# Optimization experiments

Measured on AMD Instinct MI355X. Metric: run time of the kernel, lower is better.

Reference implementation:

```python
import jax, jax.numpy as jnp
import numpy as np
import math

D = 64  # block size == head dim


def _sdpa(q, k, v):
    # q,k,v: [..., n, d]
    d = q.shape[-1]
    scores = jnp.einsum('...nd,...md->...nm', q / math.sqrt(d), k)
    probs = jax.nn.softmax(scores, axis=-1)
    return jnp.einsum('...nm,...md->...nd', probs, v)


def setup_inputs() -> dict:
    key = jax.random.key(0)
    kq, kk, kv = jax.random.split(key, 3)
    B, H, N = 4, 16, 4128  # N = 64*64 + 32 -> nonzero remainder
    q = jax.random.normal(kq, (B, H, N, D), dtype=jnp.float32)
    k = jax.random.normal(kk, (B, H, N, D), dtype=jnp.float32)
    v = jax.random.normal(kv, (B, H, N, D), dtype=jnp.float32)
    return {'q': q, 'k': k, 'v': v}


def reference(q, k, v):
    B, H, N, d = q.shape
    ND = d * (N // d)          # length covered by full DxD blocks
    h = H * (ND // d)          # total number of block-heads
    Q = q[:, :, :ND, :].reshape(B, h, d, d)
    K = k[:, :, :ND, :].reshape(B, h, d, d)
    V = v[:, :, :ND, :].reshape(B, h, d, d)
    attn_main = _sdpa(Q, K, V).reshape(B, H, ND, d)
    attn_rem = _sdpa(q[:, :, ND:, :], k[:, :, ND:, :], v[:, :, ND:, :])
    return jnp.concatenate([attn_main, attn_rem], axis=-2)
```

## Files before the change

### kernel.cpp

```cpp
#include <hip/hip_runtime.h>
#include <math.h>

#define STRH 72

typedef __attribute__((ext_vector_type(8))) short short8;
typedef __attribute__((ext_vector_type(4))) float f32x4;
typedef __attribute__((ext_vector_type(4))) short short4v;

__device__ __forceinline__ void split2(float x, unsigned short& h, unsigned short& l) {
  unsigned u = __float_as_uint(x);
  unsigned hb = (u + 0x7FFFu + ((u >> 16) & 1u)) & 0xFFFF0000u;
  h = (unsigned short)(hb >> 16);
  float r = x - __uint_as_float(hb);
  unsigned v = __float_as_uint(r);
  l = (unsigned short)((v + 0x7FFFu + ((v >> 16) & 1u)) >> 16);
}

__global__ __launch_bounds__(256, 4) void bda_kernel(
    const float* __restrict__ qg,
    const float* __restrict__ kg,
    const float* __restrict__ vg,
    float* __restrict__ og,
    int N, int nblk, int rem) {
  __shared__ unsigned short Ah[64 * STRH];
  __shared__ unsigned short Al[64 * STRH];
  __shared__ unsigned short Bh[64 * STRH];
  __shared__ unsigned short Bl[64 * STRH];

  const int wg  = blockIdx.x;
  const int blk = wg % nblk;
  const int bh  = wg / nblk;
  const int nrows = (blk == nblk - 1 && rem != 0) ? rem : 64;
  const size_t base = ((size_t)bh * (size_t)N + (size_t)blk * 64) * 64;

  const int t    = threadIdx.x;
  const int lane = t & 63;
  const int w    = t >> 6;

#pragma unroll
  for (int rnd = 0; rnd < 4; ++rnd) {
    const int e = (t << 2) + (rnd << 10);
    const int row = e >> 6, col = e & 63;
    float4 qv = make_float4(0.f, 0.f, 0.f, 0.f);
    float4 kv = qv;
    if (row < nrows) {
      qv = *(const float4*)(qg + base + e);
      kv = *(const float4*)(kg + base + e);
    }
    unsigned short qh[4], ql[4], kh[4], kl[4];
    split2(qv.x, qh[0], ql[0]); split2(qv.y, qh[1], ql[1]);
    split2(qv.z, qh[2], ql[2]); split2(qv.w, qh[3], ql[3]);
    split2(kv.x, kh[0], kl[0]); split2(kv.y, kh[1], kl[1]);
    split2(kv.z, kh[2], kl[2]); split2(kv.w, kh[3], kl[3]);
    const int a = row * STRH + col;
    *(short4v*)&Ah[a] = (short4v){(short)qh[0], (short)qh[1], (short)qh[2], (short)qh[3]};
    *(short4v*)&Al[a] = (short4v){(short)ql[0], (short)ql[1], (short)ql[2], (short)ql[3]};
    *(short4v*)&Bh[a] = (short4v){(short)kh[0], (short)kh[1], (short)kh[2], (short)kh[3]};
    *(short4v*)&Bl[a] = (short4v){(short)kl[0], (short)kl[1], (short)kl[2], (short)kl[3]};
  }

  const int vd  = t & 63;
  const int vkb = (t >> 6) * 16;
  float vr[16];
#pragma unroll
  for (int i = 0; i < 16; ++i) {
    const int k = vkb + i;
    vr[i] = (k < nrows) ? vg[base + (size_t)k * 64 + vd] : 0.f;
  }

  __syncthreads();

  const int colb = lane & 15;
  const int kofs = (lane >> 4) * 8;
  const int arow = 16 * w + colb;

  f32x4 acc[4];
#pragma unroll
  for (int i = 0; i < 4; ++i) acc[i] = (f32x4){0.f, 0.f, 0.f, 0.f};

#pragma unroll
  for (int ks = 0; ks < 2; ++ks) {
    const int kb = ks * 32 + kofs;
    const short8 ah = *(const short8*)&Ah[arow * STRH + kb];
    const short8 al = *(const short8*)&Al[arow * STRH + kb];
#pragma unroll
    for (int nt = 0; nt < 4; ++nt) {
      const int brow = 16 * nt + colb;
      const short8 bhv = *(const short8*)&Bh[brow * STRH + kb];
      const short8 blv = *(const short8*)&Bl[brow * STRH + kb];
      acc[nt] = __builtin_amdgcn_mfma_f32_16x16x32_bf16(al, bhv, acc[nt], 0, 0, 0);
      acc[nt] = __builtin_amdgcn_mfma_f32_16x16x32_bf16(ah, blv, acc[nt], 0, 0, 0);
      acc[nt] = __builtin_amdgcn_mfma_f32_16x16x32_bf16(ah, bhv, acc[nt], 0, 0, 0);
    }
  }

  const int rquad = (lane >> 4) * 4;
#pragma unroll
  for (int r = 0; r < 4; ++r) {
    const int grow = 16 * w + rquad + r;
    float s[4];
#pragma unroll
    for (int nt = 0; nt < 4; ++nt) {
      const int col = 16 * nt + colb;
      s[nt] = (col < nrows) ? acc[nt][r] * 0.125f : -1e30f;
    }
    float m = fmaxf(fmaxf(s[0], s[1]), fmaxf(s[2], s[3]));
    m = fmaxf(m, __shfl_xor(m, 1));
    m = fmaxf(m, __shfl_xor(m, 2));
    m = fmaxf(m, __shfl_xor(m, 4));
    m = fmaxf(m, __shfl_xor(m, 8));
    float p[4];
    float lsum = 0.f;
#pragma unroll
    for (int nt = 0; nt < 4; ++nt) {
      p[nt] = __expf(s[nt] - m);
      lsum += p[nt];
    }
    lsum += __shfl_xor(lsum, 1);
    lsum += __shfl_xor(lsum, 2);
    lsum += __shfl_xor(lsum, 4);
    lsum += __shfl_xor(lsum, 8);
    const float inv = 1.f / lsum;
#pragma unroll
    for (int nt = 0; nt < 4; ++nt) {
      unsigned short hh, ll;
      split2(p[nt] * inv, hh, ll);
      Ah[grow * STRH + 16 * nt + colb] = hh;
      Al[grow * STRH + 16 * nt + colb] = ll;
    }
  }

  __syncthreads();

#pragma unroll
  for (int c = 0; c < 4; ++c) {
    unsigned short h4[4], l4[4];
#pragma unroll
    for (int i = 0; i < 4; ++i) split2(vr[4 * c + i], h4[i], l4[i]);
    const int a = vd * STRH + vkb + 4 * c;
    *(short4v*)&Bh[a] = (short4v){(short)h4[0], (short)h4[1], (short)h4[2], (short)h4[3]};
    *(short4v*)&Bl[a] = (short4v){(short)l4[0], (short)l4[1], (short)l4[2], (short)l4[3]};
  }
  __syncthreads();

  f32x4 oacc[4];
#pragma unroll
  for (int i = 0; i < 4; ++i) oacc[i] = (f32x4){0.f, 0.f, 0.f, 0.f};

#pragma unroll
  for (int ks = 0; ks < 2; ++ks) {
    const int kb = ks * 32 + kofs;
    const short8 ph = *(const short8*)&Ah[arow * STRH + kb];
    const short8 pl = *(const short8*)&Al[arow * STRH + kb];
#pragma unroll
    for (int nt = 0; nt < 4; ++nt) {
      const int vrow = 16 * nt + colb;
      const short8 vh = *(const short8*)&Bh[vrow * STRH + kb];
      const short8 vl = *(const short8*)&Bl[vrow * STRH + kb];
      oacc[nt] = __builtin_amdgcn_mfma_f32_16x16x32_bf16(pl, vh, oacc[nt], 0, 0, 0);
      oacc[nt] = __builtin_amdgcn_mfma_f32_16x16x32_bf16(ph, vl, oacc[nt], 0, 0, 0);
      oacc[nt] = __builtin_amdgcn_mfma_f32_16x16x32_bf16(ph, vh, oacc[nt], 0, 0, 0);
    }
  }

#pragma unroll
  for (int nt = 0; nt < 4; ++nt) {
#pragma unroll
    for (int r = 0; r < 4; ++r) {
      const int row = 16 * w + rquad + r;
      if (row < nrows) {
        og[base + (size_t)row * 64 + 16 * nt + colb] = oacc[nt][r];
      }
    }
  }
}

extern "C" void kernel_launch(void* const* d_in, const int* in_sizes, int n_in,
                              void* d_out, int out_size, void* d_ws, size_t ws_size,
                              hipStream_t stream) {
  const float* q = (const float*)d_in[0];
  const float* k = (const float*)d_in[1];
  const float* v = (const float*)d_in[2];
  float* o = (float*)d_out;

  const int N    = 4128;
  const int BH   = in_sizes[0] / (N * 64);
  const int nblk = (N + 63) / 64;
  const int rem  = N & 63;

  bda_kernel<<<dim3(BH * nblk), dim3(256), 0, stream>>>(q, k, v, o, N, nblk, rem);
}
```

Baseline: 219.4 us.

## Use persistent workgroups with register prefetch of next block's Q/K/V

Launches a fixed grid of 1024 workgroups, each looping over a contiguous range of 64x64 blocks instead of one workgroup per block. While computing the current block, it issues global loads for the next block's Q, K and V into registers, overlapping memory latency with MFMA and softmax work. In exchange, register pressure roughly doubles for the staged tiles, which may lower occupancy under launch_bounds(256,4). It also adds an extra barrier per iteration.

```diff
diff --git a/kernel.cpp b/kernel.cpp
--- a/kernel.cpp
+++ b/kernel.cpp
@@ -2,6 +2,7 @@
 #include <math.h>
 
 #define STRH 72
+#define NWG 1024
 
 typedef __attribute__((ext_vector_type(8))) short short8;
 typedef __attribute__((ext_vector_type(4))) float f32x4;
@@ -21,156 +22,207 @@
     const float* __restrict__ kg,
     const float* __restrict__ vg,
     float* __restrict__ og,
-    int N, int nblk, int rem) {
+    int N, int nblk, int rem, int gtot) {
   __shared__ unsigned short Ah[64 * STRH];
   __shared__ unsigned short Al[64 * STRH];
   __shared__ unsigned short Bh[64 * STRH];
   __shared__ unsigned short Bl[64 * STRH];
 
-  const int wg  = blockIdx.x;
-  const int blk = wg % nblk;
-  const int bh  = wg / nblk;
-  const int nrows = (blk == nblk - 1 && rem != 0) ? rem : 64;
-  const size_t base = ((size_t)bh * (size_t)N + (size_t)blk * 64) * 64;
+  const int wg = blockIdx.x;
+  const int g0 = (wg * gtot) >> 10;
+  const int g1 = ((wg + 1) * gtot) >> 10;
 
   const int t    = threadIdx.x;
   const int lane = t & 63;
   const int w    = t >> 6;
 
-#pragma unroll
-  for (int rnd = 0; rnd < 4; ++rnd) {
-    const int e = (t << 2) + (rnd << 10);
-    const int row = e >> 6, col = e & 63;
-    float4 qv = make_float4(0.f, 0.f, 0.f, 0.f);
-    float4 kv = qv;
-    if (row < nrows) {
-      qv = *(const float4*)(qg + base + e);
-      kv = *(const float4*)(kg + base + e);
-    }
-    unsigned short qh[4], ql[4], kh[4], kl[4];
-    split2(qv.x, qh[0], ql[0]); split2(qv.y, qh[1], ql[1]);
-    split2(qv.z, qh[2], ql[2]); split2(qv.w, qh[3], ql[3]);
-    split2(kv.x, kh[0], kl[0]); split2(kv.y, kh[1], kl[1]);
-    split2(kv.z, kh[2], kl[2]); split2(kv.w, kh[3], kl[3]);
-    const int a = row * STRH + col;
-    *(short4v*)&Ah[a] = (short4v){(short)qh[0], (short)qh[1], (short)qh[2], (short)qh[3]};
-    *(short4v*)&Al[a] = (short4v){(short)ql[0], (short)ql[1], (short)ql[2], (short)ql[3]};
-    *(short4v*)&Bh[a] = (short4v){(short)kh[0], (short)kh[1], (short)kh[2], (short)kh[3]};
-    *(short4v*)&Bl[a] = (short4v){(short)kl[0], (short)kl[1], (short)kl[2], (short)kl[3]};
+  const int colb  = lane & 15;
+  const int kofs  = (lane >> 4) * 8;
+  const int arow  = 16 * w + colb;
+  const int rquad = (lane >> 4) * 4;
+  const int vd  = lane;
+  const int vkb = w * 16;
+
+  float4 qv[4], kv[4];
+  float  vr[16];
+  {
+    const int blk = g0 % nblk;
+    const int nr  = (blk == nblk - 1 && rem != 0) ? rem : 64;
+    const size_t b = ((size_t)(g0 / nblk) * (size_t)N + (size_t)blk * 64) * 64;
+#pragma unroll
+    for (int rnd = 0; rnd < 4; ++rnd) {
+      const int e = (t << 2) + (rnd << 10);
+      const int row = e >> 6;
+      qv[rnd] = make_float4(0.f, 0.f, 0.f, 0.f);
+      kv[rnd] = qv[rnd];
+      if (row < nr) {
+        qv[rnd] = *(const float4*)(qg + b + e);
+        kv[rnd] = *(const float4*)(kg + b + e);
+      }
+    }
+#pragma unroll
+    for (int i = 0; i < 16; ++i) {
+      const int k = vkb + i;
+      vr[i] = (k < nr) ? vg[b + (size_t)k * 64 + vd] : 0.f;
+    }
   }
 
-  const int vd  = t & 63;
-  const int vkb = (t >> 6) * 16;
-  float vr[16];
-#pragma unroll
-  for (int i = 0; i < 16; ++i) {
-    const int k = vkb + i;
-    vr[i] = (k < nrows) ? vg[base + (size_t)k * 64 + vd] : 0.f;
-  }
-
-  __syncthreads();
-
-  const int colb = lane & 15;
-  const int kofs = (lane >> 4) * 8;
-  const int arow = 16 * w + colb;
-
-  f32x4 acc[4];
-#pragma unroll
-  for (int i = 0; i < 4; ++i) acc[i] = (f32x4){0.f, 0.f, 0.f, 0.f};
-
-#pragma unroll
-  for (int ks = 0; ks < 2; ++ks) {
-    const int kb = ks * 32 + kofs;
-    const short8 ah = *(const short8*)&Ah[arow * STRH + kb];
-    const short8 al = *(const short8*)&Al[arow * STRH + kb];
+  for (int g = g0; g < g1; ++g) {
+    const int blk = g % nblk;
+    const int nrows = (blk == nblk - 1 && rem != 0) ? rem : 64;
+    const size_t base = ((size_t)(g / nblk) * (size_t)N + (size_t)blk * 64) * 64;
+
+    const bool more = (g + 1 < g1);
+    int nnr = 64;
+    size_t nbase = 0;
+    if (more) {
+      const int nb = (g + 1) % nblk;
+      nnr   = (nb == nblk - 1 && rem != 0) ? rem : 64;
+      nbase = ((size_t)((g + 1) / nblk) * (size_t)N + (size_t)nb * 64) * 64;
+    }
+
+#pragma unroll
+    for (int rnd = 0; rnd < 4; ++rnd) {
+      const int e = (t << 2) + (rnd << 10);
+      const int row = e >> 6, col = e & 63;
+      unsigned short qh[4], ql[4], kh[4], kl[4];
+      split2(qv[rnd].x, qh[0], ql[0]); split2(qv[rnd].y, qh[1], ql[1]);
+      split2(qv[rnd].z, qh[2], ql[2]); split2(qv[rnd].w, qh[3], ql[3]);
+      split2(kv[rnd].x, kh[0], kl[0]); split2(kv[rnd].y, kh[1], kl[1]);
+      split2(kv[rnd].z, kh[2], kl[2]); split2(kv[rnd].w, kh[3], kl[3]);
+      const int a = row * STRH + col;
+      *(short4v*)&Ah[a] = (short4v){(short)qh[0], (short)qh[1], (short)qh[2], (short)qh[3]};
+      *(short4v*)&Al[a] = (short4v){(short)ql[0], (short)ql[1], (short)ql[2], (short)ql[3]};
+      *(short4v*)&Bh[a] = (short4v){(short)kh[0], (short)kh[1], (short)kh[2], (short)kh[3]};
+      *(short4v*)&Bl[a] = (short4v){(short)kl[0], (short)kl[1], (short)kl[2], (short)kl[3]};
+    }
+
+    float4 qn[4], kn[4];
+#pragma unroll
+    for (int rnd = 0; rnd < 4; ++rnd) {
+      const int e = (t << 2) + (rnd << 10);
+      const int row = e >> 6;
+      qn[rnd] = make_float4(0.f, 0.f, 0.f, 0.f);
+      kn[rnd] = qn[rnd];
+      if (more && row < nnr) {
+        qn[rnd] = *(const float4*)(qg + nbase + e);
+        kn[rnd] = *(const float4*)(kg + nbase + e);
+      }
+    }
+
+    __syncthreads();
+
+    f32x4 acc[4];
+#pragma unroll
+    for (int i = 0; i < 4; ++i) acc[i] = (f32x4){0.f, 0.f, 0.f, 0.f};
+#pragma unroll
+    for (int ks = 0; ks < 2; ++ks) {
+      const int kb = ks * 32 + kofs;
+      const short8 ah = *(const short8*)&Ah[arow * STRH + kb];
+      const short8 al = *(const short8*)&Al[arow * STRH + kb];
+#pragma unroll
+      for (int nt = 0; nt < 4; ++nt) {
+        const int brow = 16 * nt + colb;
+        const short8 bhv = *(const short8*)&Bh[brow * STRH + kb];
+        const short8 blv = *(const short8*)&Bl[brow * STRH + kb];
+        acc[nt] = __builtin_amdgcn_mfma_f32_16x16x32_bf16(al, bhv, acc[nt], 0, 0, 0);
+        acc[nt] = __builtin_amdgcn_mfma_f32_16x16x32_bf16(ah, blv, acc[nt], 0, 0, 0);
+        acc[nt] = __builtin_amdgcn_mfma_f32_16x16x32_bf16(ah, bhv, acc[nt], 0, 0, 0);
+      }
+    }
+
+#pragma unroll
+    for (int r = 0; r < 4; ++r) {
+      const int grow = 16 * w + rquad + r;
+      float s[4];
+#pragma unroll
+      for (int nt = 0; nt < 4; ++nt) {
+        const int col = 16 * nt + colb;
+        s[nt] = (col < nrows) ? acc[nt][r] * 0.125f : -1e30f;
+      }
+      float m = fmaxf(fmaxf(s[0], s[1]), fmaxf(s[2], s[3]));
+      m = fmaxf(m, __shfl_xor(m, 1));
+      m = fmaxf(m, __shfl_xor(m, 2));
+      m = fmaxf(m, __shfl_xor(m, 4));
+      m = fmaxf(m, __shfl_xor(m, 8));
+      float p[4];
+      float lsum = 0.f;
+#pragma unroll
+      for (int nt = 0; nt < 4; ++nt) {
+        p[nt] = __expf(s[nt] - m);
+        lsum += p[nt];
+      }
+      lsum += __shfl_xor(lsum, 1);
+      lsum += __shfl_xor(lsum, 2);
+      lsum += __shfl_xor(lsum, 4);
+      lsum += __shfl_xor(lsum, 8);
+      const float inv = 1.f / lsum;
+#pragma unroll
+      for (int nt = 0; nt < 4; ++nt) {
+        unsigned short hh, ll;
+        split2(p[nt] * inv, hh, ll);
+        Ah[grow * STRH + 16 * nt + colb] = hh;
+        Al[grow * STRH + 16 * nt + colb] = ll;
+      }
+    }
+
+    __syncthreads();
+
+#pragma unroll
+    for (int c = 0; c < 4; ++c) {
+      unsigned short h4[4], l4[4];
+#pragma unroll
+      for (int i = 0; i < 4; ++i) split2(vr[4 * c + i], h4[i], l4[i]);
+      const int a = vd * STRH + vkb + 4 * c;
+      *(short4v*)&Bh[a] = (short4v){(short)h4[0], (short)h4[1], (short)h4[2], (short)h4[3]};
+      *(short4v*)&Bl[a] = (short4v){(short)l4[0], (short)l4[1], (short)l4[2], (short)l4[3]};
+    }
+
+    float vn[16];
+#pragma unroll
+    for (int i = 0; i < 16; ++i) {
+      const int k = vkb + i;
+      vn[i] = (more && k < nnr) ? vg[nbase + (size_t)k * 64 + vd] : 0.f;
+    }
+
+    __syncthreads();
+
+    f32x4 oacc[4];
+#pragma unroll
+    for (int i = 0; i < 4; ++i) oacc[i] = (f32x4){0.f, 0.f, 0.f, 0.f};
+#pragma unroll
+    for (int ks = 0; ks < 2; ++ks) {
+      const int kb = ks * 32 + kofs;
+      const short8 ph = *(const short8*)&Ah[arow * STRH + kb];
+      const short8 pl = *(const short8*)&Al[arow * STRH + kb];
+#pragma unroll
+      for (int nt = 0; nt < 4; ++nt) {
+        const int vrow = 16 * nt + colb;
+        const short8 vh = *(const short8*)&Bh[vrow * STRH + kb];
+        const short8 vl = *(const short8*)&Bl[vrow * STRH + kb];
+        oacc[nt] = __builtin_amdgcn_mfma_f32_16x16x32_bf16(pl, vh, oacc[nt], 0, 0, 0);
+        oacc[nt] = __builtin_amdgcn_mfma_f32_16x16x32_bf16(ph, vl, oacc[nt], 0, 0, 0);
+        oacc[nt] = __builtin_amdgcn_mfma_f32_16x16x32_bf16(ph, vh, oacc[nt], 0, 0, 0);
+      }
+    }
+
 #pragma unroll
     for (int nt = 0; nt < 4; ++nt) {
-      const int brow = 16 * nt + colb;
-      const short8 bhv = *(const short8*)&Bh[brow * STRH + kb];
-      const short8 blv = *(const short8*)&Bl[brow * STRH + kb];
-      acc[nt] = __builtin_amdgcn_mfma_f32_16x16x32_bf16(al, bhv, acc[nt], 0, 0, 0);
-      acc[nt] = __builtin_amdgcn_mfma_f32_16x16x32_bf16(ah, blv, acc[nt], 0, 0, 0);
-      acc[nt] = __builtin_amdgcn_mfma_f32_16x16x32_bf16(ah, bhv, acc[nt], 0, 0, 0);
-    }
-  }
-
-  const int rquad = (lane >> 4) * 4;
-#pragma unroll
-  for (int r = 0; r < 4; ++r) {
-    const int grow = 16 * w + rquad + r;
-    float s[4];
-#pragma unroll
-    for (int nt = 0; nt < 4; ++nt) {
-      const int col = 16 * nt + colb;
-      s[nt] = (col < nrows) ? acc[nt][r] * 0.125f : -1e30f;
-    }
-    float m = fmaxf(fmaxf(s[0], s[1]), fmaxf(s[2], s[3]));
-    m = fmaxf(m, __shfl_xor(m, 1));
-    m = fmaxf(m, __shfl_xor(m, 2));
-    m = fmaxf(m, __shfl_xor(m, 4));
-    m = fmaxf(m, __shfl_xor(m, 8));
-    float p[4];
-    float lsum = 0.f;
-#pragma unroll
-    for (int nt = 0; nt < 4; ++nt) {
-      p[nt] = __expf(s[nt] - m);
-      lsum += p[nt];
-    }
-    lsum += __shfl_xor(lsum, 1);
-    lsum += __shfl_xor(lsum, 2);
-    lsum += __shfl_xor(lsum, 4);
-    lsum += __shfl_xor(lsum, 8);
-    const float inv = 1.f / lsum;
-#pragma unroll
-    for (int nt = 0; nt < 4; ++nt) {
-      unsigned short hh, ll;
-      split2(p[nt] * inv, hh, ll);
-      Ah[grow * STRH + 16 * nt + colb] = hh;
-      Al[grow * STRH + 16 * nt + colb] = ll;
-    }
-  }
-
-  __syncthreads();
-
-#pragma unroll
-  for (int c = 0; c < 4; ++c) {
-    unsigned short h4[4], l4[4];
-#pragma unroll
-    for (int i = 0; i < 4; ++i) split2(vr[4 * c + i], h4[i], l4[i]);
-    const int a = vd * STRH + vkb + 4 * c;
-    *(short4v*)&Bh[a] = (short4v){(short)h4[0], (short)h4[1], (short)h4[2], (short)h4[3]};
-    *(short4v*)&Bl[a] = (short4v){(short)l4[0], (short)l4[1], (short)l4[2], (short)l4[3]};
-  }
-  __syncthreads();
-
-  f32x4 oacc[4];
-#pragma unroll
-  for (int i = 0; i < 4; ++i) oacc[i] = (f32x4){0.f, 0.f, 0.f, 0.f};
-
-#pragma unroll
-  for (int ks = 0; ks < 2; ++ks) {
-    const int kb = ks * 32 + kofs;
-    const short8 ph = *(const short8*)&Ah[arow * STRH + kb];
-    const short8 pl = *(const short8*)&Al[arow * STRH + kb];
-#pragma unroll
-    for (int nt = 0; nt < 4; ++nt) {
-      const int vrow = 16 * nt + colb;
-      const short8 vh = *(const short8*)&Bh[vrow * STRH + kb];
-      const short8 vl = *(const short8*)&Bl[vrow * STRH + kb];
-      oacc[nt] = __builtin_amdgcn_mfma_f32_16x16x32_bf16(pl, vh, oacc[nt], 0, 0, 0);
-      oacc[nt] = __builtin_amdgcn_mfma_f32_16x16x32_bf16(ph, vl, oacc[nt], 0, 0, 0);
-      oacc[nt] = __builtin_amdgcn_mfma_f32_16x16x32_bf16(ph, vh, oacc[nt], 0, 0, 0);
-    }
-  }
-
-#pragma unroll
-  for (int nt = 0; nt < 4; ++nt) {
-#pragma unroll
-    for (int r = 0; r < 4; ++r) {
-      const int row = 16 * w + rquad + r;
-      if (row < nrows) {
-        og[base + (size_t)row * 64 + 16 * nt + colb] = oacc[nt][r];
-      }
+#pragma unroll
+      for (int r = 0; r < 4; ++r) {
+        const int row = 16 * w + rquad + r;
+        if (row < nrows) {
+          og[base + (size_t)row * 64 + 16 * nt + colb] = oacc[nt][r];
+        }
+      }
+    }
+
+    if (more) {
+#pragma unroll
+      for (int i = 0; i < 4; ++i) { qv[i] = qn[i]; kv[i] = kn[i]; }
+#pragma unroll
+      for (int i = 0; i < 16; ++i) vr[i] = vn[i];
+      __syncthreads();
     }
   }
 }
@@ -187,6 +239,7 @@
   const int BH   = in_sizes[0] / (N * 64);
   const int nblk = (N + 63) / 64;
   const int rem  = N & 63;
-
-  bda_kernel<<<dim3(BH * nblk), dim3(256), 0, stream>>>(q, k, v, o, N, nblk, rem);
+  const int gtot = BH * nblk;
+
+  bda_kernel<<<dim3(NWG), dim3(256), 0, stream>>>(q, k, v, o, N, nblk, rem, gtot);
 }
```

Result: slower. 389.2 us (+77.4%).

## Load Q/K/V fragments directly from global into MFMA registers, drop LDS staging

Applied to the files above, without the earlier changes.

Q, K and V are now read from global memory straight into per-lane MFMA operand registers and split into bf16 hi/lo pairs there. This removes the Q/K/V shared-memory staging and its block-wide barriers. Only the softmax probabilities still go through LDS, and each wave reads back only rows it wrote itself, so LDS use is halved and no __syncthreads remains. In exchange, every wave re-reads the whole K and V tile from global/cache, and V is fetched with strided scalar loads. The remainder handling now depends on rem being a multiple of 16/32.

```diff
diff --git a/kernel.cpp b/kernel.cpp
--- a/kernel.cpp
+++ b/kernel.cpp
@@ -5,7 +5,6 @@
 
 typedef __attribute__((ext_vector_type(8))) short short8;
 typedef __attribute__((ext_vector_type(4))) float f32x4;
-typedef __attribute__((ext_vector_type(4))) short short4v;
 
 __device__ __forceinline__ void split2(float x, unsigned short& h, unsigned short& l) {
   unsigned u = __float_as_uint(x);
@@ -16,16 +15,24 @@
   l = (unsigned short)((v + 0x7FFFu + ((v >> 16) & 1u)) >> 16);
 }
 
+__device__ __forceinline__ void split8(const float* x, short8& h, short8& l) {
+  unsigned short hh[8], ll[8];
+#pragma unroll
+  for (int i = 0; i < 8; ++i) split2(x[i], hh[i], ll[i]);
+  h = (short8){(short)hh[0], (short)hh[1], (short)hh[2], (short)hh[3],
+               (short)hh[4], (short)hh[5], (short)hh[6], (short)hh[7]};
+  l = (short8){(short)ll[0], (short)ll[1], (short)ll[2], (short)ll[3],
+               (short)ll[4], (short)ll[5], (short)ll[6], (short)ll[7]};
+}
+
 __global__ __launch_bounds__(256, 4) void bda_kernel(
     const float* __restrict__ qg,
     const float* __restrict__ kg,
     const float* __restrict__ vg,
     float* __restrict__ og,
     int N, int nblk, int rem) {
-  __shared__ unsigned short Ah[64 * STRH];
-  __shared__ unsigned short Al[64 * STRH];
-  __shared__ unsigned short Bh[64 * STRH];
-  __shared__ unsigned short Bl[64 * STRH];
+  __shared__ unsigned short Ph[64 * STRH];
+  __shared__ unsigned short Pl[64 * STRH];
 
   const int wg  = blockIdx.x;
   const int blk = wg % nblk;
@@ -37,64 +44,49 @@
   const int lane = t & 63;
   const int w    = t >> 6;
 
+  const int colb  = lane & 15;
+  const int grp   = lane >> 4;
+  const int kofs  = grp * 8;
+  const int rquad = grp * 4;
+  const int arow  = 16 * w + colb;
+  const bool wvalid = (16 * w) < nrows;
+
+  short8 qh[2], ql[2];
 #pragma unroll
-  for (int rnd = 0; rnd < 4; ++rnd) {
-    const int e = (t << 2) + (rnd << 10);
-    const int row = e >> 6, col = e & 63;
-    float4 qv = make_float4(0.f, 0.f, 0.f, 0.f);
-    float4 kv = qv;
-    if (row < nrows) {
-      qv = *(const float4*)(qg + base + e);
-      kv = *(const float4*)(kg + base + e);
+  for (int ks = 0; ks < 2; ++ks) {
+    float qf[8];
+    if (wvalid) {
+      const float* p = qg + base + (size_t)arow * 64 + ks * 32 + kofs;
+      *(float4*)&qf[0] = *(const float4*)p;
+      *(float4*)&qf[4] = *(const float4*)(p + 4);
+    } else {
+#pragma unroll
+      for (int i = 0; i < 8; ++i) qf[i] = 0.f;
     }
-    unsigned short qh[4], ql[4], kh[4], kl[4];
-    split2(qv.x, qh[0], ql[0]); split2(qv.y, qh[1], ql[1]);
-    split2(qv.z, qh[2], ql[2]); split2(qv.w, qh[3], ql[3]);
-    split2(kv.x, kh[0], kl[0]); split2(kv.y, kh[1], kl[1]);
-    split2(kv.z, kh[2], kl[2]); split2(kv.w, kh[3], kl[3]);
-    const int a = row * STRH + col;
-    *(short4v*)&Ah[a] = (short4v){(short)qh[0], (short)qh[1], (short)qh[2], (short)qh[3]};
-    *(short4v*)&Al[a] = (short4v){(short)ql[0], (short)ql[1], (short)ql[2], (short)ql[3]};
-    *(short4v*)&Bh[a] = (short4v){(short)kh[0], (short)kh[1], (short)kh[2], (short)kh[3]};
-    *(short4v*)&Bl[a] = (short4v){(short)kl[0], (short)kl[1], (short)kl[2], (short)kl[3]};
+    split8(qf, qh[ks], ql[ks]);
   }
-
-  const int vd  = t & 63;
-  const int vkb = (t >> 6) * 16;
-  float vr[16];
-#pragma unroll
-  for (int i = 0; i < 16; ++i) {
-    const int k = vkb + i;
-    vr[i] = (k < nrows) ? vg[base + (size_t)k * 64 + vd] : 0.f;
-  }
-
-  __syncthreads();
-
-  const int colb = lane & 15;
-  const int kofs = (lane >> 4) * 8;
-  const int arow = 16 * w + colb;
 
   f32x4 acc[4];
 #pragma unroll
   for (int i = 0; i < 4; ++i) acc[i] = (f32x4){0.f, 0.f, 0.f, 0.f};
-
 #pragma unroll
-  for (int ks = 0; ks < 2; ++ks) {
-    const int kb = ks * 32 + kofs;
-    const short8 ah = *(const short8*)&Ah[arow * STRH + kb];
-    const short8 al = *(const short8*)&Al[arow * STRH + kb];
+  for (int nt = 0; nt < 4; ++nt) {
+    if (16 * nt < nrows) {
+      const float* kp = kg + base + (size_t)(16 * nt + colb) * 64 + kofs;
 #pragma unroll
-    for (int nt = 0; nt < 4; ++nt) {
-      const int brow = 16 * nt + colb;
-      const short8 bhv = *(const short8*)&Bh[brow * STRH + kb];
-      const short8 blv = *(const short8*)&Bl[brow * STRH + kb];
-      acc[nt] = __builtin_amdgcn_mfma_f32_16x16x32_bf16(al, bhv, acc[nt], 0, 0, 0);
-      acc[nt] = __builtin_amdgcn_mfma_f32_16x16x32_bf16(ah, blv, acc[nt], 0, 0, 0);
-      acc[nt] = __builtin_amdgcn_mfma_f32_16x16x32_bf16(ah, bhv, acc[nt], 0, 0, 0);
+      for (int ks = 0; ks < 2; ++ks) {
+        float kf[8];
+        *(float4*)&kf[0] = *(const float4*)(kp + ks * 32);
+        *(float4*)&kf[4] = *(const float4*)(kp + ks * 32 + 4);
+        short8 kh, kl;
+        split8(kf, kh, kl);
+        acc[nt] = __builtin_amdgcn_mfma_f32_16x16x32_bf16(ql[ks], kh, acc[nt], 0, 0, 0);
+        acc[nt] = __builtin_amdgcn_mfma_f32_16x16x32_bf16(qh[ks], kl, acc[nt], 0, 0, 0);
+        acc[nt] = __builtin_amdgcn_mfma_f32_16x16x32_bf16(qh[ks], kh, acc[nt], 0, 0, 0);
+      }
     }
   }
 
-  const int rquad = (lane >> 4) * 4;
 #pragma unroll
   for (int r = 0; r < 4; ++r) {
     const int grow = 16 * w + rquad + r;
@@ -125,51 +117,49 @@
     for (int nt = 0; nt < 4; ++nt) {
       unsigned short hh, ll;
       split2(p[nt] * inv, hh, ll);
-      Ah[grow * STRH + 16 * nt + colb] = hh;
-      Al[grow * STRH + 16 * nt + colb] = ll;
+      Ph[grow * STRH + 16 * nt + colb] = hh;
+      Pl[grow * STRH + 16 * nt + colb] = ll;
     }
   }
 
-  __syncthreads();
-
+  short8 ph[2], pl[2];
 #pragma unroll
-  for (int c = 0; c < 4; ++c) {
-    unsigned short h4[4], l4[4];
-#pragma unroll
-    for (int i = 0; i < 4; ++i) split2(vr[4 * c + i], h4[i], l4[i]);
-    const int a = vd * STRH + vkb + 4 * c;
-    *(short4v*)&Bh[a] = (short4v){(short)h4[0], (short)h4[1], (short)h4[2], (short)h4[3]};
-    *(short4v*)&Bl[a] = (short4v){(short)l4[0], (short)l4[1], (short)l4[2], (short)l4[3]};
+  for (int ks = 0; ks < 2; ++ks) {
+    ph[ks] = *(const short8*)&Ph[arow * STRH + ks * 32 + kofs];
+    pl[ks] = *(const short8*)&Pl[arow * STRH + ks * 32 + kofs];
   }
-  __syncthreads();
 
   f32x4 oacc[4];
 #pragma unroll
   for (int i = 0; i < 4; ++i) oacc[i] = (f32x4){0.f, 0.f, 0.f, 0.f};
-
 #pragma unroll
-  for (int ks = 0; ks < 2; ++ks) {
-    const int kb = ks * 32 + kofs;
-    const short8 ph = *(const short8*)&Ah[arow * STRH + kb];
-    const short8 pl = *(const short8*)&Al[arow * STRH + kb];
+  for (int nt = 0; nt < 4; ++nt) {
+    const float* vp = vg + base + 16 * nt + colb;
 #pragma unroll
-    for (int nt = 0; nt < 4; ++nt) {
-      const int vrow = 16 * nt + colb;
-      const short8 vh = *(const short8*)&Bh[vrow * STRH + kb];
-      const short8 vl = *(const short8*)&Bl[vrow * STRH + kb];
-      oacc[nt] = __builtin_amdgcn_mfma_f32_16x16x32_bf16(pl, vh, oacc[nt], 0, 0, 0);
-      oacc[nt] = __builtin_amdgcn_mfma_f32_16x16x32_bf16(ph, vl, oacc[nt], 0, 0, 0);
-      oacc[nt] = __builtin_amdgcn_mfma_f32_16x16x32_bf16(ph, vh, oacc[nt], 0, 0, 0);
+    for (int ks = 0; ks < 2; ++ks) {
+      if (ks * 32 < nrows) {
+        float vf[8];
+#pragma unroll
+        for (int j = 0; j < 8; ++j)
+          vf[j] = vp[(size_t)(ks * 32 + kofs + j) * 64];
+        short8 vh, vl;
+        split8(vf, vh, vl);
+        oacc[nt] = __builtin_amdgcn_mfma_f32_16x16x32_bf16(pl[ks], vh, oacc[nt], 0, 0, 0);
+        oacc[nt] = __builtin_amdgcn_mfma_f32_16x16x32_bf16(ph[ks], vl, oacc[nt], 0, 0, 0);
+        oacc[nt] = __builtin_amdgcn_mfma_f32_16x16x32_bf16(ph[ks], vh, oacc[nt], 0, 0, 0);
+      }
     }
   }
 
+  if (wvalid) {
 #pragma unroll
-  for (int nt = 0; nt < 4; ++nt) {
+    for (int nt = 0; nt < 4; ++nt) {
 #pragma unroll
-    for (int r = 0; r < 4; ++r) {
-      const int row = 16 * w + rquad + r;
-      if (row < nrows) {
-        og[base + (size_t)row * 64 + 16 * nt + colb] = oacc[nt][r];
+      for (int r = 0; r < 4; ++r) {
+        const int row = 16 * w + rquad + r;
+        if (row < nrows) {
+          og[base + (size_t)row * 64 + 16 * nt + colb] = oacc[nt][r];
+        }
       }
     }
   }
```

After: 226.9 us. 3.4% more time.
